# Optimization experiments

Measured on AMD Instinct MI355X. Metric: run time of the kernel, lower is better.

Reference implementation:

```python
import jax, jax.numpy as jnp
import numpy as np

HEADS = 8


def setup_inputs() -> dict:
    key = jax.random.key(0)
    ks = jax.random.split(key, 4)
    b, n, dim, inner = 8, 1024, 512, 512
    x = jax.random.normal(ks[0], (b, n, dim), jnp.float32)
    cp_mask = jax.random.randint(ks[1], (n, n), 0, 2, jnp.int32)  # binary core-periphery mask
    w_qkv = jax.random.normal(ks[2], (dim, 3 * inner), jnp.float32) * 0.02
    w_out = jax.random.normal(ks[3], (inner, dim), jnp.float32) * 0.02
    b_out = jnp.zeros((dim,), jnp.float32)
    return {"x": x, "cp_mask": cp_mask, "w_qkv": w_qkv, "w_out": w_out,
            "b_out": b_out, "patches_in_core_nodes": 16}


def reference(x, cp_mask, w_qkv, w_out, b_out, patches_in_core_nodes):
    b, n, dim = x.shape
    inner = w_qkv.shape[1] // 3
    dh = inner // HEADS
    scale = dh ** -0.5

    qkv = x @ w_qkv                                   # [b, n, 3*inner]
    q, k, v = jnp.split(qkv, 3, axis=-1)
    split_heads = lambda t: t.reshape(b, n, HEADS, dh).transpose(0, 2, 1, 3)
    q, k, v = map(split_heads, (q, k, v))             # [b, h, n, dh]

    mask = cp_mask.astype(x.dtype)                    # [n, n]
    dots_raw = jnp.einsum('bhnd,bhmd->bhnm', q, k)    # [b, h, n, n]

    # analysis pass: per-row mean |masked score|, summed over heads (detached in original)
    nnz = jnp.count_nonzero(cp_mask, axis=1).astype(x.dtype)       # [n]
    score = (jnp.abs(dots_raw * mask) * scale).sum(axis=1).sum(axis=-1) / nnz  # [b, n]
    score = jax.lax.stop_gradient(score)
    # original: list(np.argsort(score)) then list.reverse() -> batch order reversed
    idx = jnp.argsort(score, axis=-1)[::-1]           # [b, n]

    attn = jax.nn.softmax(dots_raw * scale * mask, axis=-1)
    out = jnp.einsum('bhnm,bhmd->bhnd', attn, v)      # [b, h, n, dh]
    out = out.transpose(0, 2, 1, 3).reshape(b, n, inner)

    # sequential row swap: out[j,i] <-> out[j,idx[j,i]] using the pristine clone
    out_clone = out
    bi = jnp.arange(b)
    for i in range(1, patches_in_core_nodes + 1):
        ti = idx[:, i]                                # [b]
        out = out.at[bi, i].set(out_clone[bi, ti])
        out = out.at[bi, ti].set(out_clone[:, i])
    return out @ w_out + b_out
```

## Files before the change

### kernel.cpp

```cpp
#include <hip/hip_runtime.h>
#include <hip/hip_bf16.h>

#define NN 1024
#define DH 64
#define DIM 512
#define INNER 512
#define QKV_N 1536
#define SCALE 0.125f
#define PPITCH 72

typedef short short8 __attribute__((ext_vector_type(8)));
typedef float floatx4 __attribute__((ext_vector_type(4)));

static __device__ __forceinline__ unsigned short f2bf(float x) {
  __hip_bfloat16 h = __float2bfloat16(x);
  unsigned short u;
  __builtin_memcpy(&u, &h, 2);
  return u;
}
static __device__ __forceinline__ void splitbf(float x, unsigned short& hi, unsigned short& lo) {
  __hip_bfloat16 h = __float2bfloat16(x);
  float hf = __bfloat162float(h);
  __hip_bfloat16 l = __float2bfloat16(x - hf);
  __builtin_memcpy(&hi, &h, 2);
  __builtin_memcpy(&lo, &l, 2);
}
static __device__ __forceinline__ void gll16(const unsigned short* g, unsigned short* l) {
  __builtin_amdgcn_global_load_lds(
      (const __attribute__((address_space(1))) unsigned int*)g,
      (__attribute__((address_space(3))) unsigned int*)l, 16, 0, 0);
}

__global__ __launch_bounds__(64) void nnz_kernel(const int* __restrict__ mask,
                                                 float* __restrict__ nnzf,
                                                 unsigned long long* __restrict__ Mbits) {
  int row = blockIdx.x;
  int lane = threadIdx.x;
  const int* mrow = mask + (size_t)row * NN;
  int tot = 0;
  for (int mt = 0; mt < 16; ++mt) {
    unsigned long long bits = __ballot(mrow[mt * 64 + lane] != 0);
    if (lane == 0) {
      Mbits[(size_t)mt * NN + row] = bits;
      tot += __popcll(bits);
    }
  }
  if (lane == 0) nnzf[row] = (float)tot;
}

__global__ __launch_bounds__(256) void split_kernel(const float* __restrict__ in,
                                                    unsigned short* __restrict__ hi,
                                                    unsigned short* __restrict__ lo,
                                                    int n4) {
  int i = blockIdx.x * 256 + threadIdx.x;
  if (i >= n4) return;
  float4 v = ((const float4*)in)[i];
  ushort4 h, l;
  splitbf(v.x, h.x, l.x);
  splitbf(v.y, h.y, l.y);
  splitbf(v.z, h.z, l.z);
  splitbf(v.w, h.w, l.w);
  ((ushort4*)hi)[i] = h;
  ((ushort4*)lo)[i] = l;
}

__global__ __launch_bounds__(256) void tsplit_kernel(const float* __restrict__ in, int K, int N,
                                                     unsigned short* __restrict__ hiT,
                                                     unsigned short* __restrict__ loT) {
  __shared__ float tile[32][33];
  int n0 = blockIdx.x * 32, k0 = blockIdx.y * 32;
  int t = threadIdx.x;
  int tn = t & 31, tk = t >> 5;
#pragma unroll
  for (int i = 0; i < 32; i += 8)
    tile[tk + i][tn] = in[(size_t)(k0 + tk + i) * N + n0 + tn];
  __syncthreads();
#pragma unroll
  for (int i = 0; i < 32; i += 8) {
    int n = tk + i;
    float v = tile[tn][n];
    unsigned short h, l;
    splitbf(v, h, l);
    hiT[(size_t)(n0 + n) * K + k0 + tn] = h;
    loT[(size_t)(n0 + n) * K + k0 + tn] = l;
  }
}

__global__ __launch_bounds__(256) void qkv_mfma(const unsigned short* __restrict__ xhi,
                                                const unsigned short* __restrict__ xlo,
                                                const unsigned short* __restrict__ bhiT,
                                                const unsigned short* __restrict__ bloT,
                                                unsigned short* __restrict__ qhi,
                                                unsigned short* __restrict__ qlo,
                                                unsigned short* __restrict__ khi,
                                                unsigned short* __restrict__ klo,
                                                unsigned short* __restrict__ vT) {
  __shared__ __align__(16) unsigned char smemQ[67584];
  unsigned short* planeS = (unsigned short*)smemQ;
  float* ct = (float*)smemQ;

  int l = blockIdx.x;
  int by = l & 63, bx = l >> 6;
  int r0 = by * 128, c0 = bx * 128;
  int which = c0 >> 9;
  bool split3 = (which != 2);
  int t = threadIdx.x;
  int lane = t & 63, w = t >> 6;
  int wr = w >> 1, wc = w & 1;
  int s = lane & 15, q4 = lane >> 4;
  int sx7 = s & 7;
  int r8 = lane >> 3, j7 = lane & 7;
  int colsw = ((j7 ^ r8) << 3);

  const unsigned short* gsrc;
  int tb;
  if (w == 0) { gsrc = xhi; tb = r0; }
  else if (w == 1) { gsrc = xlo; tb = r0; }
  else if (w == 2) { gsrc = bhiT; tb = c0; }
  else { gsrc = bloT; tb = c0; }
  unsigned short* lp = planeS + w * 8192;
  const unsigned short* gp = gsrc + (size_t)(tb + r8) * DIM + colsw;
  bool doStage = split3 || (w == 0) || (w == 2);

  const unsigned short* Ah = planeS;
  const unsigned short* Al = planeS + 8192;
  const unsigned short* Bh = planeS + 16384;
  const unsigned short* Bl = planeS + 24576;

  floatx4 acc[4][4];
#pragma unroll
  for (int mi = 0; mi < 4; ++mi)
#pragma unroll
    for (int ni = 0; ni < 4; ++ni) { acc[mi][ni][0] = 0.f; acc[mi][ni][1] = 0.f; acc[mi][ni][2] = 0.f; acc[mi][ni][3] = 0.f; }

  for (int kt = 0; kt < DIM; kt += 64) {
    __syncthreads();
    if (doStage) {
#pragma unroll
      for (int ii = 0; ii < 16; ++ii)
        gll16(gp + (size_t)ii * 8 * DIM + kt, lp + ii * 512);
    }
    __syncthreads();
#pragma unroll
    for (int ks2 = 0; ks2 < 2; ++ks2) {
      int pc = ((ks2 * 4 + q4) ^ sx7) << 3;
      short8 ah[4], al[4], bhf[4], blf[4];
#pragma unroll
      for (int mi = 0; mi < 4; ++mi) {
        int ra = (wr * 64 + mi * 16 + s) * 64 + pc;
        ah[mi] = *(const short8*)&Ah[ra];
        if (split3) al[mi] = *(const short8*)&Al[ra];
      }
#pragma unroll
      for (int ni = 0; ni < 4; ++ni) {
        int rb = (wc * 64 + ni * 16 + s) * 64 + pc;
        bhf[ni] = *(const short8*)&Bh[rb];
        if (split3) blf[ni] = *(const short8*)&Bl[rb];
      }
#pragma unroll
      for (int mi = 0; mi < 4; ++mi)
#pragma unroll
        for (int ni = 0; ni < 4; ++ni) {
          if (split3) {
            acc[mi][ni] = __builtin_amdgcn_mfma_f32_16x16x32_bf16(al[mi], bhf[ni], acc[mi][ni], 0, 0, 0);
            acc[mi][ni] = __builtin_amdgcn_mfma_f32_16x16x32_bf16(ah[mi], blf[ni], acc[mi][ni], 0, 0, 0);
          }
          acc[mi][ni] = __builtin_amdgcn_mfma_f32_16x16x32_bf16(ah[mi], bhf[ni], acc[mi][ni], 0, 0, 0);
        }
    }
  }

  __syncthreads();
  if (which != 2) {
    float sc = (which == 0) ? SCALE : 1.0f;
#pragma unroll
    for (int mi = 0; mi < 4; ++mi)
#pragma unroll
      for (int ni = 0; ni < 4; ++ni)
#pragma unroll
        for (int i = 0; i < 4; ++i)
          ct[(wr * 64 + mi * 16 + q4 * 4 + i) * 132 + (wc * 64 + ni * 16 + s)] = acc[mi][ni][i] * sc;
  } else {
#pragma unroll
    for (int mi = 0; mi < 4; ++mi)
#pragma unroll
      for (int ni = 0; ni < 4; ++ni)
#pragma unroll
        for (int i = 0; i < 4; ++i)
          ct[(wc * 64 + ni * 16 + s) * 132 + (wr * 64 + mi * 16 + q4 * 4 + i)] = acc[mi][ni][i];
  }
  __syncthreads();
  if (which != 2) {
    int tr = t >> 1, ch = t & 1;
    int R = r0 + tr, b = R >> 10, n = R & 1023;
    int h0 = ((c0 & 511) >> 6) + ch;
    unsigned short* dhi = (which == 0) ? qhi : khi;
    unsigned short* dlo = (which == 0) ? qlo : klo;
    size_t go = ((size_t)(((b << 3) + h0) << 10) + n) * DH;
#pragma unroll
    for (int u = 0; u < 4; ++u) {
      const float* src = &ct[tr * 132 + ch * 64 + u * 16];
      short8 h8a, h8b, l8a, l8b;
#pragma unroll
      for (int e = 0; e < 8; ++e) {
        unsigned short hh, ll;
        splitbf(src[e], hh, ll);
        h8a[e] = (short)hh; l8a[e] = (short)ll;
        splitbf(src[8 + e], hh, ll);
        h8b[e] = (short)hh; l8b[e] = (short)ll;
      }
      *(short8*)&dhi[go + u * 16] = h8a;
      *(short8*)&dhi[go + u * 16 + 8] = h8b;
      *(short8*)&dlo[go + u * 16] = l8a;
      *(short8*)&dlo[go + u * 16 + 8] = l8b;
    }
  } else {
    int cr = t >> 1, th = t & 1;
    int b = r0 >> 10;
    int hglob = ((c0 & 511) >> 6) + (cr >> 6);
    int d = cr & 63;
    int n0 = (r0 & 1023) + th * 64;
    size_t go = ((size_t)(((b << 3) + hglob) * DH) + d) * NN + n0;
#pragma unroll
    for (int u = 0; u < 4; ++u) {
      const float* src = &ct[cr * 132 + th * 64 + u * 16];
      short8 o0, o1;
#pragma unroll
      for (int e = 0; e < 8; ++e) {
        o0[e] = (short)f2bf(src[e]);
        o1[e] = (short)f2bf(src[8 + e]);
      }
      *(short8*)&vT[go + u * 16] = o0;
      *(short8*)&vT[go + u * 16 + 8] = o1;
    }
  }
}

__global__ __launch_bounds__(256, 4) void attn_kernel(const unsigned short* __restrict__ qhi,
                                                      const unsigned short* __restrict__ qlo,
                                                      const unsigned short* __restrict__ khi,
                                                      const unsigned short* __restrict__ klo,
                                                      const unsigned short* __restrict__ vT,
                                                      const unsigned long long* __restrict__ MbT,
                                                      unsigned short* __restrict__ ohi,
                                                      unsigned short* __restrict__ olo,
                                                      float* __restrict__ sph) {
  int l = blockIdx.y * 16 + blockIdx.x;
  int k = l >> 3;
  int rb = k & 15;
  int bh = (l & 7) + 8 * (k >> 4);
  int b = bh >> 3, h = bh & 7;
  int row0 = rb * 64;
  int t = threadIdx.x;
  int lane = t & 63, w = t >> 6;
  int q4 = lane >> 4, s = lane & 15;
  int sx7 = s & 7;
  int gr = 16 * w + s;
  int r8 = lane >> 3, j7 = lane & 7;
  int colsw = ((j7 ^ r8) << 3);

  __shared__ __align__(16) unsigned short stageS[3 * 4096];
  __shared__ __align__(16) unsigned short Ps[64 * PPITCH];
  __shared__ unsigned long long Mb[64];
  unsigned short* Khs = stageS;
  unsigned short* Kls = stageS + 4096;
  unsigned short* Vts = stageS + 8192;
  float* Ofl = (float*)stageS;

  const unsigned short* khp = khi + ((size_t)bh * NN + 16 * w + r8) * DH + colsw;
  const unsigned short* klp = klo + ((size_t)bh * NN + 16 * w + r8) * DH + colsw;
  const unsigned short* vtp = vT + ((size_t)bh * DH + 16 * w + r8) * NN + colsw;

  short8 aqh[2], aql[2];
  {
    size_t qb0 = ((size_t)bh * NN + row0 + gr) * DH;
#pragma unroll
    for (int ks = 0; ks < 2; ++ks) {
      aqh[ks] = *(const short8*)&qhi[qb0 + ks * 32 + q4 * 8];
      aql[ks] = *(const short8*)&qlo[qb0 + ks * 32 + q4 * 8];
    }
  }

  floatx4 Oacc[4];
  float Lacc[4], Sco[4];
#pragma unroll
  for (int j = 0; j < 4; ++j) { Oacc[j][0] = 0.f; Oacc[j][1] = 0.f; Oacc[j][2] = 0.f; Oacc[j][3] = 0.f; }
#pragma unroll
  for (int i = 0; i < 4; ++i) { Lacc[i] = 0.f; Sco[i] = 0.f; }

  for (int mt = 0; mt < 16; ++mt) {
    __syncthreads();
#pragma unroll
    for (int ii = 0; ii < 2; ++ii) {
      int lofs = (16 * w + 8 * ii) * 64;
      gll16(khp + (size_t)mt * 64 * DH + (size_t)ii * 8 * DH, Khs + lofs);
      gll16(klp + (size_t)mt * 64 * DH + (size_t)ii * 8 * DH, Kls + lofs);
      gll16(vtp + (size_t)mt * 64 + (size_t)ii * 8 * NN, Vts + lofs);
    }
    if (t < 64) Mb[t] = MbT[(size_t)mt * NN + row0 + t];
    __syncthreads();

    floatx4 Sf[4];
#pragma unroll
    for (int j = 0; j < 4; ++j) { Sf[j][0] = 0.f; Sf[j][1] = 0.f; Sf[j][2] = 0.f; Sf[j][3] = 0.f; }
#pragma unroll
    for (int ks = 0; ks < 2; ++ks) {
      int pc = ((ks * 4 + q4) ^ sx7) << 3;
#pragma unroll
      for (int j = 0; j < 4; ++j) {
        int rk = (16 * j + s) * 64 + pc;
        short8 kh8 = *(const short8*)&Khs[rk];
        short8 kl8 = *(const short8*)&Kls[rk];
        Sf[j] = __builtin_amdgcn_mfma_f32_16x16x32_bf16(aql[ks], kh8, Sf[j], 0, 0, 0);
        Sf[j] = __builtin_amdgcn_mfma_f32_16x16x32_bf16(aqh[ks], kl8, Sf[j], 0, 0, 0);
        Sf[j] = __builtin_amdgcn_mfma_f32_16x16x32_bf16(aqh[ks], kh8, Sf[j], 0, 0, 0);
      }
    }

    unsigned long long mb[4];
#pragma unroll
    for (int i = 0; i < 4; ++i) mb[i] = Mb[16 * w + 4 * q4 + i];
    unsigned short pw[4][4];
#pragma unroll
    for (int j = 0; j < 4; ++j) {
#pragma unroll
      for (int i = 0; i < 4; ++i) {
        float sv = Sf[j][i];
        float mf = ((mb[i] >> (16 * j + s)) & 1ULL) ? 1.0f : 0.0f;
        Sco[i] += fabsf(sv) * mf;
        float p = __expf(sv * mf);
        Lacc[i] += p;
        pw[i][j] = f2bf(p);
      }
    }

#pragma unroll
    for (int i = 0; i < 4; ++i)
#pragma unroll
      for (int j = 0; j < 4; ++j) Ps[(16 * w + 4 * q4 + i) * PPITCH + 16 * j + s] = pw[i][j];

#pragma unroll
    for (int ks = 0; ks < 2; ++ks) {
      int mm0 = ks * 32 + q4 * 8;
      short8 ap = *(const short8*)&Ps[gr * PPITCH + mm0];
      int pc = ((ks * 4 + q4) ^ sx7) << 3;
#pragma unroll
      for (int j = 0; j < 4; ++j) {
        short8 bv = *(const short8*)&Vts[(16 * j + s) * 64 + pc];
        Oacc[j] = __builtin_amdgcn_mfma_f32_16x16x32_bf16(ap, bv, Oacc[j], 0, 0, 0);
      }
    }
  }

#pragma unroll
  for (int off = 1; off < 16; off <<= 1) {
#pragma unroll
    for (int i = 0; i < 4; ++i) {
      Lacc[i] += __shfl_xor(Lacc[i], off, 16);
      Sco[i] += __shfl_xor(Sco[i], off, 16);
    }
  }
  if (s == 0) {
#pragma unroll
    for (int i = 0; i < 4; ++i)
      sph[((size_t)bh << 10) + row0 + 16 * w + 4 * q4 + i] = Sco[i];
  }

  __syncthreads();
#pragma unroll
  for (int i = 0; i < 4; ++i) {
    float iv = 1.0f / Lacc[i];
#pragma unroll
    for (int j = 0; j < 4; ++j)
      Ofl[(16 * w + 4 * q4 + i) * 68 + 16 * j + s] = Oacc[j][i] * iv;
  }
  __syncthreads();
  {
    int tr = t >> 2, dq = t & 3;
    int r = row0 + tr;
    size_t go = ((size_t)((b << 10) + r)) * INNER + (h << 6) + dq * 16;
    const float* src = &Ofl[tr * 68 + dq * 16];
    short8 h8a, h8b, l8a, l8b;
#pragma unroll
    for (int e = 0; e < 8; ++e) {
      unsigned short hh, ll;
      splitbf(src[e], hh, ll);
      h8a[e] = (short)hh; l8a[e] = (short)ll;
      splitbf(src[8 + e], hh, ll);
      h8b[e] = (short)hh; l8b[e] = (short)ll;
    }
    *(short8*)&ohi[go] = h8a;
    *(short8*)&ohi[go + 8] = h8b;
    *(short8*)&olo[go] = l8a;
    *(short8*)&olo[go + 8] = l8b;
  }
}

__global__ __launch_bounds__(256) void score_select(const float* __restrict__ sph,
                                                    const float* __restrict__ nnzf,
                                                    const int* __restrict__ pic_ptr,
                                                    int* __restrict__ asc) {
  int bb = blockIdx.x;
  int t = threadIdx.x;
  int cnt = pic_ptr[0] + 1;
  float v[4];
#pragma unroll
  for (int i = 0; i < 4; ++i) {
    int r = t + 256 * i;
    float sv = 0.f;
#pragma unroll
    for (int h = 0; h < 8; ++h) sv += sph[(size_t)(((bb << 3) + h) << 10) + r];
    v[i] = sv / nnzf[r];
  }
  __shared__ float wv[4];
  __shared__ int wi[4];
  __shared__ int bsel;
  for (int sel = 0; sel < cnt; ++sel) {
    float bv = v[0];
    int bi = t;
#pragma unroll
    for (int i = 1; i < 4; ++i) {
      if (v[i] < bv) { bv = v[i]; bi = t + 256 * i; }
    }
#pragma unroll
    for (int off = 1; off < 64; off <<= 1) {
      float ov = __shfl_xor(bv, off, 64);
      int oi = __shfl_xor(bi, off, 64);
      if (ov < bv || (ov == bv && oi < bi)) { bv = ov; bi = oi; }
    }
    if ((t & 63) == 0) { wv[t >> 6] = bv; wi[t >> 6] = bi; }
    __syncthreads();
    if (t == 0) {
      float B = wv[0]; int I = wi[0];
#pragma unroll
      for (int q = 1; q < 4; ++q) {
        if (wv[q] < B || (wv[q] == B && wi[q] < I)) { B = wv[q]; I = wi[q]; }
      }
      bsel = I;
      asc[bb * 32 + sel] = I;
    }
    __syncthreads();
    int wloc = bsel - t;
    if (wloc >= 0 && (wloc & 255) == 0 && wloc < 1024) v[wloc >> 8] = 3.4e38f;
    __syncthreads();
  }
}

__global__ __launch_bounds__(256) void build_src(const int* __restrict__ asc,
                                                 const int* __restrict__ pic_ptr,
                                                 int* __restrict__ src) {
  int bi = blockIdx.x;
  int t = threadIdx.x;
  for (int r = t; r < 1024; r += 256) src[bi * 1024 + r] = r;
  __syncthreads();
  if (t == 0) {
    int pic = pic_ptr[0];
    const int* a = &asc[(7 - bi) * 32];
    for (int i = 1; i <= pic; ++i) {
      int ti = a[i];
      src[bi * 1024 + i] = ti;
      src[bi * 1024 + ti] = i;
    }
  }
}

__global__ __launch_bounds__(256) void out_mfma(const unsigned short* __restrict__ ahi,
                                                const unsigned short* __restrict__ alo,
                                                const unsigned short* __restrict__ bhiT,
                                                const unsigned short* __restrict__ bloT,
                                                const float* __restrict__ bias,
                                                const int* __restrict__ src,
                                                float* __restrict__ C) {
  __shared__ __align__(16) unsigned short planeS[4 * 8192];
  int l = blockIdx.x;
  int by = l & 63, bx = l >> 6;
  int r0 = by * 128, c0 = bx * 128;
  int t = threadIdx.x;
  int lane = t & 63, w = t >> 6;
  int wr = w >> 1, wc = w & 1;
  int s = lane & 15, q4 = lane >> 4;
  int sx7 = s & 7;
  int r8 = lane >> 3, j7 = lane & 7;
  int colsw = ((j7 ^ r8) << 3);
  int bb1024 = (r0 >> 10) << 10;

  int srcrow[16];
  if (w < 2) {
#pragma unroll
    for (int ii = 0; ii < 16; ++ii) srcrow[ii] = src[r0 + ii * 8 + r8];
  }
  const unsigned short* gsrc = (w == 0) ? ahi : (w == 1) ? alo : (w == 2) ? bhiT : bloT;
  unsigned short* lp = planeS + w * 8192;

  const unsigned short* Ah = planeS;
  const unsigned short* Al = planeS + 8192;
  const unsigned short* Bh = planeS + 16384;
  const unsigned short* Bl = planeS + 24576;

  floatx4 acc[4][4];
#pragma unroll
  for (int mi = 0; mi < 4; ++mi)
#pragma unroll
    for (int ni = 0; ni < 4; ++ni) { acc[mi][ni][0] = 0.f; acc[mi][ni][1] = 0.f; acc[mi][ni][2] = 0.f; acc[mi][ni][3] = 0.f; }

  for (int kt = 0; kt < INNER; kt += 64) {
    __syncthreads();
    if (w < 2) {
#pragma unroll
      for (int ii = 0; ii < 16; ++ii)
        gll16(gsrc + (size_t)(bb1024 + srcrow[ii]) * INNER + kt + colsw, lp + ii * 512);
    } else {
#pragma unroll
      for (int ii = 0; ii < 16; ++ii)
        gll16(gsrc + (size_t)(c0 + ii * 8 + r8) * INNER + kt + colsw, lp + ii * 512);
    }
    __syncthreads();
#pragma unroll
    for (int ks2 = 0; ks2 < 2; ++ks2) {
      int pc = ((ks2 * 4 + q4) ^ sx7) << 3;
      short8 ah[4], al[4], bhf[4], blf[4];
#pragma unroll
      for (int mi = 0; mi < 4; ++mi) {
        int ra = (wr * 64 + mi * 16 + s) * 64 + pc;
        ah[mi] = *(const short8*)&Ah[ra];
        al[mi] = *(const short8*)&Al[ra];
      }
#pragma unroll
      for (int ni = 0; ni < 4; ++ni) {
        int rb = (wc * 64 + ni * 16 + s) * 64 + pc;
        bhf[ni] = *(const short8*)&Bh[rb];
        blf[ni] = *(const short8*)&Bl[rb];
      }
#pragma unroll
      for (int mi = 0; mi < 4; ++mi)
#pragma unroll
        for (int ni = 0; ni < 4; ++ni) {
          acc[mi][ni] = __builtin_amdgcn_mfma_f32_16x16x32_bf16(al[mi], bhf[ni], acc[mi][ni], 0, 0, 0);
          acc[mi][ni] = __builtin_amdgcn_mfma_f32_16x16x32_bf16(ah[mi], blf[ni], acc[mi][ni], 0, 0, 0);
          acc[mi][ni] = __builtin_amdgcn_mfma_f32_16x16x32_bf16(ah[mi], bhf[ni], acc[mi][ni], 0, 0, 0);
        }
    }
  }

#pragma unroll
  for (int ni = 0; ni < 4; ++ni) {
    int Cl = c0 + wc * 64 + ni * 16 + s;
    float bv = bias[Cl];
#pragma unroll
    for (int mi = 0; mi < 4; ++mi)
#pragma unroll
      for (int i = 0; i < 4; ++i) {
        int R = r0 + wr * 64 + mi * 16 + q4 * 4 + i;
        C[(size_t)R * DIM + Cl] = acc[mi][ni][i] + bv;
      }
  }
}

extern "C" void kernel_launch(void* const* d_in, const int* in_sizes, int n_in,
                              void* d_out, int out_size, void* d_ws, size_t ws_size,
                              hipStream_t stream) {
  const float* x      = (const float*)d_in[0];
  const int*   cpmask = (const int*)d_in[1];
  const float* w_qkv  = (const float*)d_in[2];
  const float* w_out  = (const float*)d_in[3];
  const float* b_out  = (const float*)d_in[4];
  const int*   pic    = (const int*)d_in[5];
  float* out = (float*)d_out;

  unsigned short* xhi   = (unsigned short*)d_ws;
  unsigned short* xlo   = xhi + 4194304;
  unsigned short* wqhiT = xlo + 4194304;
  unsigned short* wqloT = wqhiT + 786432;
  unsigned short* wohiT = wqloT + 786432;
  unsigned short* woloT = wohiT + 262144;
  unsigned short* qhi   = woloT + 262144;
  unsigned short* qlo   = qhi + 4194304;
  unsigned short* khi   = qlo + 4194304;
  unsigned short* klo   = khi + 4194304;
  unsigned short* vbp   = klo + 4194304;
  float* sph  = (float*)(vbp + 4194304);
  float* sc   = sph + 65536;
  float* nnzf = sc + 8192;
  int*   asc  = (int*)(nnzf + 1024);
  int*   src  = asc + 512;
  unsigned long long* Mbits = (unsigned long long*)(src + 8192);
  unsigned short* vTp = (unsigned short*)(Mbits + 16384);

  unsigned short* ohi = xhi;
  unsigned short* olo = xlo;

  hipLaunchKernelGGL(nnz_kernel,    dim3(1024),    dim3(64),  0, stream, cpmask, nnzf, Mbits);
  hipLaunchKernelGGL(split_kernel,  dim3(4096),    dim3(256), 0, stream, x, xhi, xlo, 1048576);
  hipLaunchKernelGGL(tsplit_kernel, dim3(48, 16),  dim3(256), 0, stream, w_qkv, DIM, QKV_N, wqhiT, wqloT);
  hipLaunchKernelGGL(tsplit_kernel, dim3(16, 16),  dim3(256), 0, stream, w_out, INNER, DIM, wohiT, woloT);
  hipLaunchKernelGGL(qkv_mfma,      dim3(768),     dim3(256), 0, stream, xhi, xlo, wqhiT, wqloT,
                     qhi, qlo, khi, klo, vTp);
  hipLaunchKernelGGL(attn_kernel,   dim3(16, 64),  dim3(256), 0, stream, qhi, qlo, khi, klo, vTp,
                     Mbits, ohi, olo, sph);
  hipLaunchKernelGGL(score_select,  dim3(8),       dim3(256), 0, stream, sph, nnzf, pic, asc);
  hipLaunchKernelGGL(build_src,     dim3(8),       dim3(256), 0, stream, asc, pic, src);
  hipLaunchKernelGGL(out_mfma,      dim3(256),     dim3(256), 0, stream, ohi, olo, wohiT, woloT,
                     b_out, src, out);
}
```

Baseline: 226.5 us.

## Fuse prep kernels, halve GEMM LDS staging, fold log2e into Q scale, merge select

Merges the nnz, split and transpose-split kernels into one prep launch, and the score-select and build-src kernels into a single one-wave kernel, cutting the launch count. The QKV and output GEMMs now stage only one operand in LDS and read the other straight from global memory, which halves shared-memory use and may raise occupancy at the cost of uncoalesced direct loads. The QKV epilogue writes its tile in two halves to fit the smaller LDS. Q is prescaled by scale*log2(e) so the attention kernel can use exp2f, and the mask bit handling is simplified.

```diff
diff --git a/kernel.cpp b/kernel.cpp
--- a/kernel.cpp
+++ b/kernel.cpp
@@ -6,7 +6,7 @@
 #define DIM 512
 #define INNER 512
 #define QKV_N 1536
-#define SCALE 0.125f
+#define QPRESCALE 0.1803368801111244f
 #define PPITCH 72
 
 typedef short short8 __attribute__((ext_vector_type(8)));
@@ -31,58 +31,71 @@
       (__attribute__((address_space(3))) unsigned int*)l, 16, 0, 0);
 }
 
-__global__ __launch_bounds__(64) void nnz_kernel(const int* __restrict__ mask,
-                                                 float* __restrict__ nnzf,
-                                                 unsigned long long* __restrict__ Mbits) {
-  int row = blockIdx.x;
-  int lane = threadIdx.x;
-  const int* mrow = mask + (size_t)row * NN;
-  int tot = 0;
-  for (int mt = 0; mt < 16; ++mt) {
-    unsigned long long bits = __ballot(mrow[mt * 64 + lane] != 0);
-    if (lane == 0) {
-      Mbits[(size_t)mt * NN + row] = bits;
-      tot += __popcll(bits);
-    }
-  }
-  if (lane == 0) nnzf[row] = (float)tot;
-}
-
-__global__ __launch_bounds__(256) void split_kernel(const float* __restrict__ in,
-                                                    unsigned short* __restrict__ hi,
-                                                    unsigned short* __restrict__ lo,
-                                                    int n4) {
-  int i = blockIdx.x * 256 + threadIdx.x;
-  if (i >= n4) return;
-  float4 v = ((const float4*)in)[i];
-  ushort4 h, l;
-  splitbf(v.x, h.x, l.x);
-  splitbf(v.y, h.y, l.y);
-  splitbf(v.z, h.z, l.z);
-  splitbf(v.w, h.w, l.w);
-  ((ushort4*)hi)[i] = h;
-  ((ushort4*)lo)[i] = l;
-}
-
-__global__ __launch_bounds__(256) void tsplit_kernel(const float* __restrict__ in, int K, int N,
-                                                     unsigned short* __restrict__ hiT,
-                                                     unsigned short* __restrict__ loT) {
+__global__ __launch_bounds__(256) void prep_kernel(const float* __restrict__ x,
+                                                   const float* __restrict__ w_qkv,
+                                                   const float* __restrict__ w_out,
+                                                   const int* __restrict__ mask,
+                                                   unsigned short* __restrict__ xhi,
+                                                   unsigned short* __restrict__ xlo,
+                                                   unsigned short* __restrict__ wqhiT,
+                                                   unsigned short* __restrict__ wqloT,
+                                                   unsigned short* __restrict__ wohiT,
+                                                   unsigned short* __restrict__ woloT,
+                                                   float* __restrict__ nnzf,
+                                                   unsigned long long* __restrict__ Mbits) {
   __shared__ float tile[32][33];
-  int n0 = blockIdx.x * 32, k0 = blockIdx.y * 32;
+  int blk = blockIdx.x;
   int t = threadIdx.x;
-  int tn = t & 31, tk = t >> 5;
-#pragma unroll
-  for (int i = 0; i < 32; i += 8)
-    tile[tk + i][tn] = in[(size_t)(k0 + tk + i) * N + n0 + tn];
-  __syncthreads();
-#pragma unroll
-  for (int i = 0; i < 32; i += 8) {
-    int n = tk + i;
-    float v = tile[tn][n];
-    unsigned short h, l;
-    splitbf(v, h, l);
-    hiT[(size_t)(n0 + n) * K + k0 + tn] = h;
-    loT[(size_t)(n0 + n) * K + k0 + tn] = l;
+  if (blk < 4096) {
+    int i = blk * 256 + t;
+    float4 v = ((const float4*)x)[i];
+    ushort4 h, l;
+    splitbf(v.x, h.x, l.x);
+    splitbf(v.y, h.y, l.y);
+    splitbf(v.z, h.z, l.z);
+    splitbf(v.w, h.w, l.w);
+    ((ushort4*)xhi)[i] = h;
+    ((ushort4*)xlo)[i] = l;
+  } else if (blk < 5120) {
+    const float* in;
+    unsigned short *hiT, *loT;
+    int K = 512, N, n0, k0;
+    if (blk < 4864) {
+      int idx = blk - 4096;
+      in = w_qkv; hiT = wqhiT; loT = wqloT; N = QKV_N;
+      n0 = (idx % 48) * 32; k0 = (idx / 48) * 32;
+    } else {
+      int idx = blk - 4864;
+      in = w_out; hiT = wohiT; loT = woloT; N = DIM;
+      n0 = (idx % 16) * 32; k0 = (idx / 16) * 32;
+    }
+    int tn = t & 31, tk = t >> 5;
+#pragma unroll
+    for (int i = 0; i < 32; i += 8)
+      tile[tk + i][tn] = in[(size_t)(k0 + tk + i) * N + n0 + tn];
+    __syncthreads();
+#pragma unroll
+    for (int i = 0; i < 32; i += 8) {
+      int n = tk + i;
+      float v = tile[tn][n];
+      unsigned short h, l;
+      splitbf(v, h, l);
+      hiT[(size_t)(n0 + n) * K + k0 + tn] = h;
+      loT[(size_t)(n0 + n) * K + k0 + tn] = l;
+    }
+  } else {
+    int row = (blk - 5120) * 4 + (t >> 6);
+    int lane = t & 63;
+    const int* mrow = mask + (size_t)row * NN;
+    int tot = 0;
+    for (int mt = 0; mt < 16; ++mt) {
+      unsigned long long bits = __ballot(mrow[mt * 64 + lane] != 0);
+      if (lane == 0) {
+        Mbits[(size_t)mt * NN + row] = bits;
+        tot += __popcll(bits);
+      }
+    }
+    if (lane == 0) nnzf[row] = (float)tot;
   }
 }
 
@@ -95,8 +108,9 @@
                                                 unsigned short* __restrict__ khi,
                                                 unsigned short* __restrict__ klo,
                                                 unsigned short* __restrict__ vT) {
-  __shared__ __align__(16) unsigned char smemQ[67584];
-  unsigned short* planeS = (unsigned short*)smemQ;
+  __shared__ __align__(16) unsigned char smemQ[33792];
+  unsigned short* Bh = (unsigned short*)smemQ;
+  unsigned short* Bl = Bh + 8192;
   float* ct = (float*)smemQ;
 
   int l = blockIdx.x;
@@ -112,20 +126,10 @@
   int r8 = lane >> 3, j7 = lane & 7;
   int colsw = ((j7 ^ r8) << 3);
 
-  const unsigned short* gsrc;
-  int tb;
-  if (w == 0) { gsrc = xhi; tb = r0; }
-  else if (w == 1) { gsrc = xlo; tb = r0; }
-  else if (w == 2) { gsrc = bhiT; tb = c0; }
-  else { gsrc = bloT; tb = c0; }
-  unsigned short* lp = planeS + w * 8192;
-  const unsigned short* gp = gsrc + (size_t)(tb + r8) * DIM + colsw;
-  bool doStage = split3 || (w == 0) || (w == 2);
-
-  const unsigned short* Ah = planeS;
-  const unsigned short* Al = planeS + 8192;
-  const unsigned short* Bh = planeS + 16384;
-  const unsigned short* Bl = planeS + 24576;
+  const unsigned short* aHb = xhi + (size_t)(r0 + wr * 64 + s) * DIM + q4 * 8;
+  const unsigned short* aLb = xlo + (size_t)(r0 + wr * 64 + s) * DIM + q4 * 8;
+  const unsigned short* gBh = bhiT + (size_t)(c0 + 32 * w + r8) * DIM + colsw;
+  const unsigned short* gBl = bloT + (size_t)(c0 + 32 * w + r8) * DIM + colsw;
 
   floatx4 acc[4][4];
 #pragma unroll
@@ -135,21 +139,22 @@
 
   for (int kt = 0; kt < DIM; kt += 64) {
     __syncthreads();
-    if (doStage) {
-#pragma unroll
-      for (int ii = 0; ii < 16; ++ii)
-        gll16(gp + (size_t)ii * 8 * DIM + kt, lp + ii * 512);
+#pragma unroll
+    for (int ii = 0; ii < 4; ++ii) {
+      int lofs = (32 * w + 8 * ii) * 64;
+      gll16(gBh + (size_t)ii * 8 * DIM + kt, Bh + lofs);
+      if (split3) gll16(gBl + (size_t)ii * 8 * DIM + kt, Bl + lofs);
     }
     __syncthreads();
 #pragma unroll
     for (int ks2 = 0; ks2 < 2; ++ks2) {
       int pc = ((ks2 * 4 + q4) ^ sx7) << 3;
+      int ko = kt + ks2 * 32;
       short8 ah[4], al[4], bhf[4], blf[4];
 #pragma unroll
       for (int mi = 0; mi < 4; ++mi) {
-        int ra = (wr * 64 + mi * 16 + s) * 64 + pc;
-        ah[mi] = *(const short8*)&Ah[ra];
-        if (split3) al[mi] = *(const short8*)&Al[ra];
+        ah[mi] = *(const short8*)(aHb + (size_t)mi * 16 * DIM + ko);
+        if (split3) al[mi] = *(const short8*)(aLb + (size_t)mi * 16 * DIM + ko);
       }
 #pragma unroll
       for (int ni = 0; ni < 4; ++ni) {
@@ -170,68 +175,78 @@
     }
   }
 
+  int b = r0 >> 10;
   __syncthreads();
   if (which != 2) {
-    float sc = (which == 0) ? SCALE : 1.0f;
-#pragma unroll
-    for (int mi = 0; mi < 4; ++mi)
-#pragma unroll
-      for (int ni = 0; ni < 4; ++ni)
-#pragma unroll
-        for (int i = 0; i < 4; ++i)
-          ct[(wr * 64 + mi * 16 + q4 * 4 + i) * 132 + (wc * 64 + ni * 16 + s)] = acc[mi][ni][i] * sc;
-  } else {
-#pragma unroll
-    for (int mi = 0; mi < 4; ++mi)
-#pragma unroll
-      for (int ni = 0; ni < 4; ++ni)
-#pragma unroll
-        for (int i = 0; i < 4; ++i)
-          ct[(wc * 64 + ni * 16 + s) * 132 + (wr * 64 + mi * 16 + q4 * 4 + i)] = acc[mi][ni][i];
-  }
-  __syncthreads();
-  if (which != 2) {
-    int tr = t >> 1, ch = t & 1;
-    int R = r0 + tr, b = R >> 10, n = R & 1023;
-    int h0 = ((c0 & 511) >> 6) + ch;
+    float scf = (which == 0) ? QPRESCALE : 1.0f;
     unsigned short* dhi = (which == 0) ? qhi : khi;
     unsigned short* dlo = (which == 0) ? qlo : klo;
-    size_t go = ((size_t)(((b << 3) + h0) << 10) + n) * DH;
-#pragma unroll
-    for (int u = 0; u < 4; ++u) {
-      const float* src = &ct[tr * 132 + ch * 64 + u * 16];
-      short8 h8a, h8b, l8a, l8b;
-#pragma unroll
-      for (int e = 0; e < 8; ++e) {
-        unsigned short hh, ll;
-        splitbf(src[e], hh, ll);
-        h8a[e] = (short)hh; l8a[e] = (short)ll;
-        splitbf(src[8 + e], hh, ll);
-        h8b[e] = (short)hh; l8b[e] = (short)ll;
-      }
-      *(short8*)&dhi[go + u * 16] = h8a;
-      *(short8*)&dhi[go + u * 16 + 8] = h8b;
-      *(short8*)&dlo[go + u * 16] = l8a;
-      *(short8*)&dlo[go + u * 16 + 8] = l8b;
+    int hb = (c0 & 511) >> 6;
+#pragma unroll
+    for (int p = 0; p < 2; ++p) {
+      if (p) __syncthreads();
+      if (wr == p) {
+#pragma unroll
+        for (int mi = 0; mi < 4; ++mi)
+#pragma unroll
+          for (int ni = 0; ni < 4; ++ni)
+#pragma unroll
+            for (int i = 0; i < 4; ++i)
+              ct[(mi * 16 + q4 * 4 + i) * 132 + (wc * 64 + ni * 16 + s)] = acc[mi][ni][i] * scf;
+      }
+      __syncthreads();
+      {
+        int tr = t >> 2, seg = t & 3;
+        int h = hb + (seg >> 1);
+        int d0 = (seg & 1) * 32;
+        int n = (r0 & 1023) + 64 * p + tr;
+        size_t go = ((size_t)(((b << 3) + h) << 10) + n) * DH + d0;
+        const float* src = &ct[tr * 132 + seg * 32];
+        short8 h8[4], l8[4];
+#pragma unroll
+        for (int u = 0; u < 4; ++u)
+#pragma unroll
+          for (int e = 0; e < 8; ++e) {
+            unsigned short hh, ll;
+            splitbf(src[u * 8 + e], hh, ll);
+            h8[u][e] = (short)hh; l8[u][e] = (short)ll;
+          }
+#pragma unroll
+        for (int u = 0; u < 4; ++u) {
+          *(short8*)&dhi[go + u * 8] = h8[u];
+          *(short8*)&dlo[go + u * 8] = l8[u];
+        }
+      }
     }
   } else {
-    int cr = t >> 1, th = t & 1;
-    int b = r0 >> 10;
-    int hglob = ((c0 & 511) >> 6) + (cr >> 6);
-    int d = cr & 63;
-    int n0 = (r0 & 1023) + th * 64;
-    size_t go = ((size_t)(((b << 3) + hglob) * DH) + d) * NN + n0;
-#pragma unroll
-    for (int u = 0; u < 4; ++u) {
-      const float* src = &ct[cr * 132 + th * 64 + u * 16];
-      short8 o0, o1;
-#pragma unroll
-      for (int e = 0; e < 8; ++e) {
-        o0[e] = (short)f2bf(src[e]);
-        o1[e] = (short)f2bf(src[8 + e]);
-      }
-      *(short8*)&vT[go + u * 16] = o0;
-      *(short8*)&vT[go + u * 16 + 8] = o1;
+    int hb = (c0 & 511) >> 6;
+#pragma unroll
+    for (int p = 0; p < 2; ++p) {
+      if (p) __syncthreads();
+      if (wc == p) {
+#pragma unroll
+        for (int mi = 0; mi < 4; ++mi)
+#pragma unroll
+          for (int ni = 0; ni < 4; ++ni)
+#pragma unroll
+            for (int i = 0; i < 4; ++i)
+              ct[(ni * 16 + s) * 132 + (wr * 64 + mi * 16 + q4 * 4 + i)] = acc[mi][ni][i];
+      }
+      __syncthreads();
+      {
+        int d = t >> 2, nseg = t & 3;
+        int h = hb + p;
+        int n0 = (r0 & 1023) + nseg * 32;
+        size_t go = ((size_t)(((b << 3) + h) * DH) + d) * NN + n0;
+        const float* src = &ct[d * 132 + nseg * 32];
+        short8 o[4];
+#pragma unroll
+        for (int u = 0; u < 4; ++u)
+#pragma unroll
+          for (int e = 0; e < 8; ++e) o[u][e] = (short)f2bf(src[u * 8 + e]);
+#pragma unroll
+        for (int u = 0; u < 4; ++u) *(short8*)&vT[go + u * 8] = o[u];
+      }
     }
   }
 }
@@ -317,18 +332,16 @@
       }
     }
 
-    unsigned long long mb[4];
-#pragma unroll
-    for (int i = 0; i < 4; ++i) mb[i] = Mb[16 * w + 4 * q4 + i];
     unsigned short pw[4][4];
 #pragma unroll
-    for (int j = 0; j < 4; ++j) {
-#pragma unroll
-      for (int i = 0; i < 4; ++i) {
+    for (int i = 0; i < 4; ++i) {
+      unsigned long long u = Mb[16 * w + 4 * q4 + i] >> s;
+#pragma unroll
+      for (int j = 0; j < 4; ++j) {
         float sv = Sf[j][i];
-        float mf = ((mb[i] >> (16 * j + s)) & 1ULL) ? 1.0f : 0.0f;
-        Sco[i] += fabsf(sv) * mf;
-        float p = __expf(sv * mf);
+        float tv = ((u >> (16 * j)) & 1ULL) ? sv : 0.0f;
+        Sco[i] += fabsf(tv);
+        float p = exp2f(tv);
         Lacc[i] += p;
         pw[i][j] = f2bf(p);
       }
@@ -341,8 +354,7 @@
 
 #pragma unroll
     for (int ks = 0; ks < 2; ++ks) {
-      int mm0 = ks * 32 + q4 * 8;
-      short8 ap = *(const short8*)&Ps[gr * PPITCH + mm0];
+      short8 ap = *(const short8*)&Ps[gr * PPITCH + ks * 32 + q4 * 8];
       int pc = ((ks * 4 + q4) ^ sx7) << 3;
 #pragma unroll
       for (int j = 0; j < 4; ++j) {
@@ -396,31 +408,33 @@
   }
 }
 
-__global__ __launch_bounds__(256) void score_select(const float* __restrict__ sph,
-                                                    const float* __restrict__ nnzf,
-                                                    const int* __restrict__ pic_ptr,
-                                                    int* __restrict__ asc) {
+__global__ __launch_bounds__(64) void sel_build(const float* __restrict__ sph,
+                                                const float* __restrict__ nnzf,
+                                                const int* __restrict__ pic_ptr,
+                                                int* __restrict__ src) {
   int bb = blockIdx.x;
-  int t = threadIdx.x;
-  int cnt = pic_ptr[0] + 1;
-  float v[4];
-#pragma unroll
-  for (int i = 0; i < 4; ++i) {
-    int r = t + 256 * i;
+  int lane = threadIdx.x;
+  int pic = pic_ptr[0];
+  int cnt = pic + 1;
+  int ob = 7 - bb;
+  float v[16];
+#pragma unroll
+  for (int i = 0; i < 16; ++i) {
+    int r = i * 64 + lane;
     float sv = 0.f;
 #pragma unroll
     for (int h = 0; h < 8; ++h) sv += sph[(size_t)(((bb << 3) + h) << 10) + r];
     v[i] = sv / nnzf[r];
   }
-  __shared__ float wv[4];
-  __shared__ int wi[4];
-  __shared__ int bsel;
+#pragma unroll
+  for (int i = 0; i < 16; ++i) src[ob * 1024 + i * 64 + lane] = i * 64 + lane;
   for (int sel = 0; sel < cnt; ++sel) {
     float bv = v[0];
-    int bi = t;
-#pragma unroll
-    for (int i = 1; i < 4; ++i) {
-      if (v[i] < bv) { bv = v[i]; bi = t + 256 * i; }
+    int bi = lane;
+#pragma unroll
+    for (int i = 1; i < 16; ++i) {
+      int r = i * 64 + lane;
+      if (v[i] < bv) { bv = v[i]; bi = r; }
     }
 #pragma unroll
     for (int off = 1; off < 64; off <<= 1) {
@@ -428,38 +442,15 @@
       int oi = __shfl_xor(bi, off, 64);
       if (ov < bv || (ov == bv && oi < bi)) { bv = ov; bi = oi; }
     }
-    if ((t & 63) == 0) { wv[t >> 6] = bv; wi[t >> 6] = bi; }
-    __syncthreads();
-    if (t == 0) {
-      float B = wv[0]; int I = wi[0];
-#pragma unroll
-      for (int q = 1; q < 4; ++q) {
-        if (wv[q] < B || (wv[q] == B && wi[q] < I)) { B = wv[q]; I = wi[q]; }
-      }
-      bsel = I;
-      asc[bb * 32 + sel] = I;
-    }
-    __syncthreads();
-    int wloc = bsel - t;
-    if (wloc >= 0 && (wloc & 255) == 0 && wloc < 1024) v[wloc >> 8] = 3.4e38f;
-    __syncthreads();
-  }
-}
-
-__global__ __launch_bounds__(256) void build_src(const int* __restrict__ asc,
-                                                 const int* __restrict__ pic_ptr,
-                                                 int* __restrict__ src) {
-  int bi = blockIdx.x;
-  int t = threadIdx.x;
-  for (int r = t; r < 1024; r += 256) src[bi * 1024 + r] = r;
-  __syncthreads();
-  if (t == 0) {
-    int pic = pic_ptr[0];
-    const int* a = &asc[(7 - bi) * 32];
-    for (int i = 1; i <= pic; ++i) {
-      int ti = a[i];
-      src[bi * 1024 + i] = ti;
-      src[bi * 1024 + ti] = i;
+    if ((bi & 63) == lane) {
+      int slot = bi >> 6;
+#pragma unroll
+      for (int i = 0; i < 16; ++i)
+        if (i == slot) v[i] = 3.4e38f;
+    }
+    if (sel >= 1 && lane == 0) {
+      src[ob * 1024 + sel] = bi;
+      src[ob * 1024 + bi] = sel;
     }
   }
 }
@@ -471,7 +462,7 @@
                                                 const float* __restrict__ bias,
                                                 const int* __restrict__ src,
                                                 float* __restrict__ C) {
-  __shared__ __align__(16) unsigned short planeS[4 * 8192];
+  __shared__ __align__(16) unsigned short planeS[2 * 8192];
   int l = blockIdx.x;
   int by = l & 63, bx = l >> 6;
   int r0 = by * 128, c0 = bx * 128;
@@ -484,18 +475,16 @@
   int colsw = ((j7 ^ r8) << 3);
   int bb1024 = (r0 >> 10) << 10;
 
-  int srcrow[16];
-  if (w < 2) {
-#pragma unroll
-    for (int ii = 0; ii < 16; ++ii) srcrow[ii] = src[r0 + ii * 8 + r8];
-  }
-  const unsigned short* gsrc = (w == 0) ? ahi : (w == 1) ? alo : (w == 2) ? bhiT : bloT;
-  unsigned short* lp = planeS + w * 8192;
-
-  const unsigned short* Ah = planeS;
-  const unsigned short* Al = planeS + 8192;
-  const unsigned short* Bh = planeS + 16384;
-  const unsigned short* Bl = planeS + 24576;
+  unsigned short* Ah = planeS;
+  unsigned short* Al = planeS + 8192;
+
+  int grow[4];
+#pragma unroll
+  for (int ii = 0; ii < 4; ++ii)
+    grow[ii] = bb1024 + src[r0 + 32 * w + 8 * ii + r8];
+
+  const unsigned short* bHb = bhiT + (size_t)(c0 + wc * 64 + s) * INNER + q4 * 8;
+  const unsigned short* bLb = bloT + (size_t)(c0 + wc * 64 + s) * INNER + q4 * 8;
 
   floatx4 acc[4][4];
 #pragma unroll
@@ -505,19 +494,17 @@
 
   for (int kt = 0; kt < INNER; kt += 64) {
     __syncthreads();
-    if (w < 2) {
-#pragma unroll
-      for (int ii = 0; ii < 16; ++ii)
-        gll16(gsrc + (size_t)(bb1024 + srcrow[ii]) * INNER + kt + colsw, lp + ii * 512);
-    } else {
-#pragma unroll
-      for (int ii = 0; ii < 16; ++ii)
-        gll16(gsrc + (size_t)(c0 + ii * 8 + r8) * INNER + kt + colsw, lp + ii * 512);
+#pragma unroll
+    for (int ii = 0; ii < 4; ++ii) {
+      int lofs = (32 * w + 8 * ii) * 64;
+      gll16(ahi + (size_t)grow[ii] * INNER + kt + colsw, Ah + lofs);
+      gll16(alo + (size_t)grow[ii] * INNER + kt + colsw, Al + lofs);
     }
     __syncthreads();
 #pragma unroll
     for (int ks2 = 0; ks2 < 2; ++ks2) {
       int pc = ((ks2 * 4 + q4) ^ sx7) << 3;
+      int ko = kt + ks2 * 32;
       short8 ah[4], al[4], bhf[4], blf[4];
 #pragma unroll
       for (int mi = 0; mi < 4; ++mi) {
@@ -527,9 +514,8 @@
       }
 #pragma unroll
       for (int ni = 0; ni < 4; ++ni) {
-        int rb = (wc * 64 + ni * 16 + s) * 64 + pc;
-        bhf[ni] = *(const short8*)&Bh[rb];
-        blf[ni] = *(const short8*)&Bl[rb];
+        bhf[ni] = *(const short8*)(bHb + (size_t)ni * 16 * INNER + ko);
+        blf[ni] = *(const short8*)(bLb + (size_t)ni * 16 * INNER + ko);
       }
 #pragma unroll
       for (int mi = 0; mi < 4; ++mi)
@@ -589,16 +575,13 @@
   unsigned short* ohi = xhi;
   unsigned short* olo = xlo;
 
-  hipLaunchKernelGGL(nnz_kernel,    dim3(1024),    dim3(64),  0, stream, cpmask, nnzf, Mbits);
-  hipLaunchKernelGGL(split_kernel,  dim3(4096),    dim3(256), 0, stream, x, xhi, xlo, 1048576);
-  hipLaunchKernelGGL(tsplit_kernel, dim3(48, 16),  dim3(256), 0, stream, w_qkv, DIM, QKV_N, wqhiT, wqloT);
-  hipLaunchKernelGGL(tsplit_kernel, dim3(16, 16),  dim3(256), 0, stream, w_out, INNER, DIM, wohiT, woloT);
-  hipLaunchKernelGGL(qkv_mfma,      dim3(768),     dim3(256), 0, stream, xhi, xlo, wqhiT, wqloT,
+  hipLaunchKernelGGL(prep_kernel, dim3(5376),   dim3(256), 0, stream,
+                     x, w_qkv, w_out, cpmask, xhi, xlo, wqhiT, wqloT, wohiT, woloT, nnzf, Mbits);
+  hipLaunchKernelGGL(qkv_mfma,    dim3(768),    dim3(256), 0, stream, xhi, xlo, wqhiT, wqloT,
                      qhi, qlo, khi, klo, vTp);
-  hipLaunchKernelGGL(attn_kernel,   dim3(16, 64),  dim3(256), 0, stream, qhi, qlo, khi, klo, vTp,
+  hipLaunchKernelGGL(attn_kernel, dim3(16, 64), dim3(256), 0, stream, qhi, qlo, khi, klo, vTp,
                      Mbits, ohi, olo, sph);
-  hipLaunchKernelGGL(score_select,  dim3(8),       dim3(256), 0, stream, sph, nnzf, pic, asc);
-  hipLaunchKernelGGL(build_src,     dim3(8),       dim3(256), 0, stream, asc, pic, src);
-  hipLaunchKernelGGL(out_mfma,      dim3(256),     dim3(256), 0, stream, ohi, olo, wohiT, woloT,
+  hipLaunchKernelGGL(sel_build,   dim3(8),      dim3(64),  0, stream, sph, nnzf, pic, src);
+  hipLaunchKernelGGL(out_mfma,    dim3(256),    dim3(256), 0, stream, ohi, olo, wohiT, woloT,
                      b_out, src, out);
 }
```

Result: slower. 244.7 us (+8.0%).
